# Optimization experiments

Hardware: AMD Instinct MI355X
Metric: run time of the kernel (lower is better)

Reference implementation:

```python
import jax, jax.numpy as jnp
import numpy as np

PI = 3.1415  # the module hard-codes 3.1415, not math.pi


def setup_inputs() -> dict:
    nt, ns, nh, ng = 1000, 1024, 64, 32
    key = jax.random.key(0)
    kP, kE, kT1, kT2, kxc, kW, kb = jax.random.split(key, 7)
    # physically plausible forcings: P, E >= 0; T2 > T1 always
    P = jax.random.uniform(kP, (nt, ns)) * 10.0
    E = jax.random.uniform(kE, (nt, ns)) * 5.0
    T1 = jax.random.normal(kT1, (nt, ns)) * 10.0
    T2 = T1 + jax.random.uniform(kT2, (nt, ns)) * 10.0 + 0.1
    x = jnp.stack([P, E, T1, T2], axis=-1)  # [nt, ns, 4]
    xc = jax.random.normal(kxc, (ns, ng))
    std = 1.0 / np.sqrt(nh)  # reset_parameters: uniform(-std, std)
    W3 = jax.random.uniform(kW, (nh * 4, ng), minval=-std, maxval=std)
    b3 = jax.random.uniform(kb, (nh * 4,), minval=-std, maxval=std)
    return {"x": x, "xc": xc, "W3": W3, "b3": b3}


def reference(x, xc, W3, b3):
    nh = W3.shape[0] // 4
    P, E, T1, T2 = x[..., 0], x[..., 1], x[..., 2], x[..., 3]  # each [nt, ns]
    Ta = (T1 + T2) * 0.5
    melted = T1 >= 0.0
    frozen = T2 <= 0.0
    masked = melted | frozen
    # NaN-safe arccos: out-of-range args occur exactly where masked overrides apply
    arg = jnp.where(masked, 0.0, jnp.clip((T1 + T2) / (T2 - T1), -1.0, 1.0))
    rP = 1.0 - jnp.arccos(arg) / PI
    rP = jnp.where(melted, 1.0, jnp.where(frozen, 0.0, rP))
    Ps = (1.0 - rP) * P  # snow fraction
    Pl = rP * P          # liquid fraction
    # static gates (fc3 on catchment attributes); dropout is identity in eval
    w = xc @ W3.T + b3  # [ns, 4*nh]
    gm = jnp.exp(w[:, :nh]) + 1.0
    ge = jax.nn.sigmoid(w[:, nh:2 * nh])
    go = jax.nn.sigmoid(w[:, 2 * nh:3 * nh])
    ga = jax.nn.softmax(w[:, 3 * nh:], axis=1)

    ns = P.shape[1]
    S0 = jnp.zeros((ns, nh), dtype=x.dtype)
    H0 = jnp.zeros((ns, nh), dtype=x.dtype)

    def step(carry, inp):
        S0, H0 = carry
        Ps_k, Pl_k, E_k, Ta_k = inp  # each [ns]
        Sm = jnp.minimum(S0, jax.nn.relu(Ta_k[:, None] * gm))  # snowmelt
        S = S0 + Ps_k[:, None]
        H = jax.nn.relu(H0 + Sm + Pl_k[:, None] - E_k[:, None] * ge)
        Q = H * go
        Y = jnp.sum(Q * ga, axis=1)  # [ns]
        return (S - Sm, H - Q), Y

    _, Yout = jax.lax.scan(step, (S0, H0), (Ps, Pl, E, Ta))
    return Yout  # [nt, ns]
```

## Files before the change

### kernel.cpp

```cpp
#include <hip/hip_runtime.h>
#include <math.h>

#define NH 64
#define NG 32
#define LROW (NH + 1)

__device__ __forceinline__ float bcast(float v, int l) {
    return __int_as_float(__builtin_amdgcn_readlane(__float_as_int(v), l));
}

__global__ __launch_bounds__(64) void waternet_kernel(
    const float* __restrict__ x,
    const float* __restrict__ xc,
    const float* __restrict__ W3,
    const float* __restrict__ b3,
    float* __restrict__ out,
    int nt, int ns)
{
    const int b    = blockIdx.x;
    const int s    = (b & 7) * (ns >> 3) + (b >> 3);
    const int lane = threadIdx.x;

    __shared__ float ybuf[2][NH * LROW];

    float wq[4];
    #pragma unroll
    for (int q = 0; q < 4; ++q) {
        const float4* row = reinterpret_cast<const float4*>(W3 + (size_t)(q * NH + lane) * NG);
        const float4* xr  = reinterpret_cast<const float4*>(xc + (size_t)s * NG);
        float a = 0.f;
        #pragma unroll
        for (int g = 0; g < NG / 4; ++g) {
            const float4 w  = row[g];
            const float4 xv = xr[g];
            a = fmaf(w.x, xv.x, a); a = fmaf(w.y, xv.y, a);
            a = fmaf(w.z, xv.z, a); a = fmaf(w.w, xv.w, a);
        }
        wq[q] = a + b3[q * NH + lane];
    }
    const float gm = expf(wq[0]) + 1.0f;
    const float ge = 1.0f / (1.0f + expf(-wq[1]));
    const float go = 1.0f / (1.0f + expf(-wq[2]));
    float mx = wq[3];
    #pragma unroll
    for (int o = 32; o; o >>= 1) mx = fmaxf(mx, __shfl_xor(mx, o, 64));
    const float ex = expf(wq[3] - mx);
    float smx = ex;
    #pragma unroll
    for (int o = 32; o; o >>= 1) smx += __shfl_xor(smx, o, 64);
    const float ga = ex / smx;
    const float gq = go * ga;
    const float gk = 1.0f - go;

    float S = 0.f, H = 0.f;
    const int nchunk = (nt + NH - 1) / NH;

    int tp = min(lane, nt - 1);
    float4 f = *reinterpret_cast<const float4*>(x + ((size_t)tp * ns + s) * 4);

    for (int c = 0; c < nchunk; ++c) {
        const int t0  = c * NH;
        const int cnt = min(NH, nt - t0);

        const float P = f.x, E = f.y, T1 = f.z, T2 = f.w;
        const float Ta  = 0.5f * (T1 + T2);
        const float arg = fminf(1.f, fmaxf(-1.f, (T1 + T2) / (T2 - T1)));
        const float r   = 1.f - acosf(arg) * (1.0f / 3.1415f);
        const float rP  = (T1 >= 0.f) ? 1.f : ((T2 <= 0.f) ? 0.f : r);
        const float Ps  = (1.f - rP) * P;
        const float Pl  = rP * P;
        const float Tr  = fmaxf(Ta, 0.f);

        tp = min(t0 + NH + lane, nt - 1);
        const float4 fn = *reinterpret_cast<const float4*>(x + ((size_t)tp * ns + s) * 4);

        float* yb = ybuf[c & 1];

        #define STEP(J) { \
            const float Trj = bcast(Tr, (J)); \
            const float Psj = bcast(Ps, (J)); \
            const float Plj = bcast(Pl, (J)); \
            const float Ej  = bcast(E,  (J)); \
            const float Sm  = fminf(S, Trj * gm);             \
            const float A   = fmaf(-Ej, ge, Plj);             \
            const float Hn  = fmaxf(H + A + Sm, 0.f);         \
            S = (S + Psj) - Sm; \
            H = Hn * gk; \
            yb[(J) * LROW + lane] = Hn * gq; \
        }

        if (cnt == NH) {
            #pragma unroll
            for (int j = 0; j < NH; ++j) STEP(j)
        } else {
            for (int j = 0; j < cnt; ++j) STEP(j)
        }
        #undef STEP

        if (lane < cnt) {
            const float* row = &yb[lane * LROW];
            float y0 = 0.f, y1 = 0.f, y2 = 0.f, y3 = 0.f;
            #pragma unroll
            for (int g = 0; g < NH; g += 4) {
                y0 += row[g + 0]; y1 += row[g + 1];
                y2 += row[g + 2]; y3 += row[g + 3];
            }
            out[(size_t)(t0 + lane) * ns + s] = (y0 + y1) + (y2 + y3);
        }

        f = fn;
    }
}

extern "C" void kernel_launch(void* const* d_in, const int* in_sizes, int n_in,
                              void* d_out, int out_size, void* d_ws, size_t ws_size,
                              hipStream_t stream) {
    const float* x  = (const float*)d_in[0];
    const float* xc = (const float*)d_in[1];
    const float* W3 = (const float*)d_in[2];
    const float* b3 = (const float*)d_in[3];
    float* out = (float*)d_out;

    const int nh = in_sizes[3] / 4;
    const int ng = in_sizes[2] / (4 * nh);
    const int ns = in_sizes[1] / ng;
    const int nt = in_sizes[0] / (ns * 4);

    waternet_kernel<<<dim3(ns), dim3(64), 0, stream>>>(x, xc, W3, b3, out, nt, ns);
}
```

Before: 111.5 us.

## Pipeline chunk reduction into next chunk's recurrence and use LDS scalar broadcast

Moves each chunk's per-timestep forcings into shared memory as float4 and reads them with uniform LDS loads, replacing four readlane broadcasts per step. The row-sum reduction of the previous chunk is interleaved into the current chunk's unrolled recurrence with vectorized float4 reads, using a padded row stride of 68, so the reduction latency overlaps the serial chain. acosf is replaced with a polynomial approximation. The changes add pipeline prologue and epilogue code paths and small accuracy differences from the approximate arccos. There is also no barrier between the scal writes and the broadcast reads, which relies on the block being a single wavefront.

```diff
diff --git a/kernel.cpp b/kernel.cpp
--- a/kernel.cpp
+++ b/kernel.cpp
@@ -3,11 +3,7 @@
 
 #define NH 64
 #define NG 32
-#define LROW (NH + 1)
-
-__device__ __forceinline__ float bcast(float v, int l) {
-    return __int_as_float(__builtin_amdgcn_readlane(__float_as_int(v), l));
-}
+#define LROW 68
 
 __global__ __launch_bounds__(64) void waternet_kernel(
     const float* __restrict__ x,
@@ -21,7 +17,8 @@
     const int s    = (b & 7) * (ns >> 3) + (b >> 3);
     const int lane = threadIdx.x;
 
-    __shared__ float ybuf[2][NH * LROW];
+    __shared__ float yb[2][NH * LROW];
+    __shared__ float scal[NH * 4];
 
     float wq[4];
     #pragma unroll
@@ -53,63 +50,95 @@
     const float gk = 1.0f - go;
 
     float S = 0.f, H = 0.f;
-    const int nchunk = (nt + NH - 1) / NH;
+    const int nfull = nt / NH;
+    const int tail  = nt - nfull * NH;
 
     int tp = min(lane, nt - 1);
     float4 f = *reinterpret_cast<const float4*>(x + ((size_t)tp * ns + s) * 4);
 
-    for (int c = 0; c < nchunk; ++c) {
-        const int t0  = c * NH;
-        const int cnt = min(NH, nt - t0);
+    #define PHASE_A() { \
+        const float P = f.x, E = f.y, T1 = f.z, T2 = f.w; \
+        const float Ta  = 0.5f * (T1 + T2); \
+        const float arg = fminf(1.f, fmaxf(-1.f, (T1 + T2) / (T2 - T1))); \
+        const float aa  = fabsf(arg); \
+        float p = fmaf(aa, -0.0012624911f, 0.0066700901f); \
+        p = fmaf(aa, p, -0.0170881256f); p = fmaf(aa, p, 0.0308918810f); \
+        p = fmaf(aa, p, -0.0501743046f); p = fmaf(aa, p, 0.0889789874f); \
+        p = fmaf(aa, p, -0.2145988016f); p = fmaf(aa, p, 1.5707963050f); \
+        const float rr0 = sqrtf(1.f - aa) * p;                   \
+        const float ac  = (arg >= 0.f) ? rr0 : (3.14159265358979f - rr0); \
+        const float rr  = 1.f - ac * (1.0f / 3.1415f);           \
+        const float rP  = (T1 >= 0.f) ? 1.f : ((T2 <= 0.f) ? 0.f : rr); \
+        float4 st; st.x = fmaxf(Ta, 0.f); st.y = (1.f - rP) * P; \
+        st.z = rP * P;  st.w = E; \
+        *reinterpret_cast<float4*>(&scal[lane * 4]) = st; \
+    }
 
-        const float P = f.x, E = f.y, T1 = f.z, T2 = f.w;
-        const float Ta  = 0.5f * (T1 + T2);
-        const float arg = fminf(1.f, fmaxf(-1.f, (T1 + T2) / (T2 - T1)));
-        const float r   = 1.f - acosf(arg) * (1.0f / 3.1415f);
-        const float rP  = (T1 >= 0.f) ? 1.f : ((T2 <= 0.f) ? 0.f : r);
-        const float Ps  = (1.f - rP) * P;
-        const float Pl  = rP * P;
-        const float Tr  = fmaxf(Ta, 0.f);
+    #define STEP_BODY(sc, YB, J) { \
+        const float M   = sc.x * gm;                      \
+        const float Sm  = fminf(S, M);                    \
+        const float tmp = fmaf(-sc.w, ge, sc.z);          \
+        const float Hn  = fmaxf(H + Sm + tmp, 0.f); \
+        S = (S + sc.y) - Sm; \
+        H = Hn * gk; \
+        (YB)[(J) * LROW + lane] = Hn * gq; \
+    }
 
-        tp = min(t0 + NH + lane, nt - 1);
+    for (int c = 0; c < nfull; ++c) {
+        PHASE_A();
+
+        tp = min((c + 1) * NH + lane, nt - 1);
         const float4 fn = *reinterpret_cast<const float4*>(x + ((size_t)tp * ns + s) * 4);
 
-        float* yb = ybuf[c & 1];
+        float*       ybw = yb[c & 1];
+        const float* ybr = yb[(c & 1) ^ 1];
+        float z0 = 0.f, z1 = 0.f, z2 = 0.f, z3 = 0.f;
 
-        #define STEP(J) { \
-            const float Trj = bcast(Tr, (J)); \
-            const float Psj = bcast(Ps, (J)); \
-            const float Plj = bcast(Pl, (J)); \
-            const float Ej  = bcast(E,  (J)); \
-            const float Sm  = fminf(S, Trj * gm);             \
-            const float A   = fmaf(-Ej, ge, Plj);             \
-            const float Hn  = fmaxf(H + A + Sm, 0.f);         \
-            S = (S + Psj) - Sm; \
-            H = Hn * gk; \
-            yb[(J) * LROW + lane] = Hn * gq; \
+        #pragma unroll
+        for (int j = 0; j < NH; ++j) {
+            const float4 sc = *reinterpret_cast<const float4*>(&scal[j * 4]);
+            STEP_BODY(sc, ybw, j)
+            if ((j & 3) == 1) {
+                const float4 v = *reinterpret_cast<const float4*>(&ybr[lane * LROW + (j >> 2) * 4]);
+                z0 += v.x; z1 += v.y; z2 += v.z; z3 += v.w;
+            }
         }
-
-        if (cnt == NH) {
-            #pragma unroll
-            for (int j = 0; j < NH; ++j) STEP(j)
-        } else {
-            for (int j = 0; j < cnt; ++j) STEP(j)
-        }
-        #undef STEP
-
-        if (lane < cnt) {
-            const float* row = &yb[lane * LROW];
-            float y0 = 0.f, y1 = 0.f, y2 = 0.f, y3 = 0.f;
-            #pragma unroll
-            for (int g = 0; g < NH; g += 4) {
-                y0 += row[g + 0]; y1 += row[g + 1];
-                y2 += row[g + 2]; y3 += row[g + 3];
-            }
-            out[(size_t)(t0 + lane) * ns + s] = (y0 + y1) + (y2 + y3);
-        }
-
+        if (c > 0)
+            out[(size_t)((c - 1) * NH + lane) * ns + s] = (z0 + z1) + (z2 + z3);
         f = fn;
     }
+
+    if (nfull > 0) {
+        const float* row = &yb[(nfull - 1) & 1][lane * LROW];
+        float z0 = 0.f, z1 = 0.f, z2 = 0.f, z3 = 0.f;
+        #pragma unroll
+        for (int g = 0; g < NH / 4; ++g) {
+            const float4 v = *reinterpret_cast<const float4*>(&row[g * 4]);
+            z0 += v.x; z1 += v.y; z2 += v.z; z3 += v.w;
+        }
+        out[(size_t)((nfull - 1) * NH + lane) * ns + s] = (z0 + z1) + (z2 + z3);
+    }
+
+    if (tail > 0) {
+        PHASE_A();
+        float* ybw = yb[nfull & 1];
+        for (int j = 0; j < tail; ++j) {
+            const float4 sc = *reinterpret_cast<const float4*>(&scal[j * 4]);
+            STEP_BODY(sc, ybw, j)
+        }
+        if (lane < tail) {
+            const float* row = &ybw[lane * LROW];
+            float z0 = 0.f, z1 = 0.f, z2 = 0.f, z3 = 0.f;
+            #pragma unroll
+            for (int g = 0; g < NH / 4; ++g) {
+                const float4 v = *reinterpret_cast<const float4*>(&row[g * 4]);
+                z0 += v.x; z1 += v.y; z2 += v.z; z3 += v.w;
+            }
+            out[(size_t)(nfull * NH + lane) * ns + s] = (z0 + z1) + (z2 + z3);
+        }
+    }
+    #undef PHASE_A
+    #undef STEP_BODY
 }
 
 extern "C" void kernel_launch(void* const* d_in, const int* in_sizes, int n_in,
```

Result: no change. 111.6 us (+0.1%).
